# Performance work log

Hardware: AMD Instinct MI355X
Metric: run time of the kernel (lower is better)

The kernel has to match this reference:

```python
import jax, jax.numpy as jnp
import numpy as np

B, N = 2, 512
NEG = -1e9  # mask fill for masked max (self-loops guarantee >=1 neighbor)


def _dense_init(key, fan_in, fan_out):
    kw, kb = jax.random.split(key)
    scale = 1.0 / np.sqrt(fan_in)
    W = jax.random.normal(kw, (fan_in, fan_out), dtype=jnp.float32) * scale
    b = jnp.zeros((fan_out,), dtype=jnp.float32)
    return W, b


def setup_inputs() -> dict:
    key = jax.random.key(0)
    ks = jax.random.split(key, 16)
    coordinates = jax.random.normal(ks[0], (B, N, 3), dtype=jnp.float32)
    adjacency = (jax.random.uniform(ks[1], (B, N, N)) < 0.05).astype(jnp.float32)
    adjacency = jnp.maximum(adjacency, jnp.eye(N, dtype=jnp.float32)[None])
    node_features = jax.random.normal(ks[2], (B, N, 63), dtype=jnp.float32)
    center_scores = jax.random.uniform(ks[3], (B, N, 1), dtype=jnp.float32)

    W_h1, b_h1 = _dense_init(ks[4], 3, 64)
    W_h2, b_h2 = _dense_init(ks[5], 64, 64)
    # concat dim = 64 + 63 + 1 = 128; EdgeConv edge feature dim = 2 * F_in
    ec1_W1, ec1_b1 = _dense_init(ks[6], 256, 64)
    ec1_W2, ec1_b2 = _dense_init(ks[7], 64, 64)
    ec2_W1, ec2_b1 = _dense_init(ks[8], 128, 64)
    ec2_W2, ec2_b2 = _dense_init(ks[9], 64, 64)
    ec3_W1, ec3_b1 = _dense_init(ks[10], 128, 64)
    ec3_W2, ec3_b2 = _dense_init(ks[11], 64, 64)
    W_h6, b_h6 = _dense_init(ks[12], 64, 128)
    W_out, b_out = _dense_init(ks[13], 128, 3)
    return dict(coordinates=coordinates, adjacency=adjacency,
                node_features=node_features, center_scores=center_scores,
                W_h1=W_h1, b_h1=b_h1, W_h2=W_h2, b_h2=b_h2,
                ec1_W1=ec1_W1, ec1_b1=ec1_b1, ec1_W2=ec1_W2, ec1_b2=ec1_b2,
                ec2_W1=ec2_W1, ec2_b1=ec2_b1, ec2_W2=ec2_W2, ec2_b2=ec2_b2,
                ec3_W1=ec3_W1, ec3_b1=ec3_b1, ec3_W2=ec3_W2, ec3_b2=ec3_b2,
                W_h6=W_h6, b_h6=b_h6, W_out=W_out, b_out=b_out)


def _edge_conv(A, x, W1, b1, W2, b2):
    # DGCNN EdgeConv: m_ij = MLP([x_i, x_j - x_i]); out_i = max_{j in N(i)} m_ij
    Bn, Nn, F = x.shape
    xi = jnp.broadcast_to(x[:, :, None, :], (Bn, Nn, Nn, F))  # [B,N,N,F]
    xj = jnp.broadcast_to(x[:, None, :, :], (Bn, Nn, Nn, F))
    e = jnp.concatenate([xi, xj - xi], axis=-1)               # [B,N,N,2F]
    h = jax.nn.relu(jnp.einsum('bijf,fo->bijo', e, W1) + b1)
    h = jax.nn.relu(jnp.einsum('bijo,op->bijp', h, W2) + b2)
    h = jnp.where(A[..., None] > 0, h, NEG)
    return jnp.max(h, axis=2)                                  # [B,N,F_out]


def reference(coordinates, adjacency, node_features, center_scores,
              W_h1, b_h1, W_h2, b_h2,
              ec1_W1, ec1_b1, ec1_W2, ec1_b2,
              ec2_W1, ec2_b1, ec2_W2, ec2_b2,
              ec3_W1, ec3_b1, ec3_W2, ec3_b2,
              W_h6, b_h6, W_out, b_out):
    x = jax.nn.relu(coordinates @ W_h1 + b_h1)
    x = jax.nn.relu(x @ W_h2 + b_h2)
    x = jnp.concatenate([x, node_features, center_scores], axis=-1)  # [B,N,128]
    x = _edge_conv(adjacency, x, ec1_W1, ec1_b1, ec1_W2, ec1_b2)
    ec1_out = x
    x = _edge_conv(adjacency, x, ec2_W1, ec2_b1, ec2_W2, ec2_b2)
    ec2_out = x
    x = x + ec1_out
    x = _edge_conv(adjacency, x, ec3_W1, ec3_b1, ec3_W2, ec3_b2)
    x = x + ec2_out
    x = jax.nn.relu(x @ W_h6 + b_h6)
    x = jax.nn.relu(x @ W_out + b_out)
    return x
```

## Files before the change

### kernel.cpp

```cpp
#include <hip/hip_runtime.h>
#include <hip/hip_bf16.h>


#define NEGV -1e9f
#define MAXNBR 96

__device__ __forceinline__ float edge_partial(
    int beg, int myc, int o, const int* nbr, const float* __restrict__ vb,
    float ui, float bo, const float* wcol, float* hbuf) {
  float acc = NEGV;
  if (myc <= 0) return acc;
  float vl[4];
#pragma unroll
  for (int t = 0; t < 4; t++) {
    int e = t < myc ? t : myc - 1;
    vl[t] = vb[nbr[beg + e] * 64 + o];
  }
  for (int e0 = 0; e0 < myc; e0 += 4) {
    float4 hw;
    hw.x = fmaxf(ui + vl[0], 0.f);
    hw.y = fmaxf(ui + vl[1], 0.f);
    hw.z = fmaxf(ui + vl[2], 0.f);
    hw.w = fmaxf(ui + vl[3], 0.f);
    *(float4*)(hbuf + o * 4) = hw;
    if (e0 + 4 < myc) {
#pragma unroll
      for (int t = 0; t < 4; t++) {
        int e = e0 + 4 + t;
        if (e >= myc) e = myc - 1;
        vl[t] = vb[nbr[beg + e] * 64 + o];
      }
    }
    float s0 = bo, s1 = bo, s2 = bo, s3 = bo;
#pragma unroll
    for (int k = 0; k < 64; k++) {
      float4 hv = *(const float4*)(hbuf + k * 4);
      s0 = fmaf(hv.x, wcol[k], s0);
      s1 = fmaf(hv.y, wcol[k], s1);
      s2 = fmaf(hv.z, wcol[k], s2);
      s3 = fmaf(hv.w, wcol[k], s3);
    }
    acc = fmaxf(acc, fmaxf(s0, 0.f));
    if (e0 + 1 < myc) acc = fmaxf(acc, fmaxf(s1, 0.f));
    if (e0 + 2 < myc) acc = fmaxf(acc, fmaxf(s2, 0.f));
    if (e0 + 3 < myc) acc = fmaxf(acc, fmaxf(s3, 0.f));
  }
  return acc;
}

__global__ __launch_bounds__(64) void k1_node_uv(
    const float* __restrict__ coords, const float* __restrict__ A,
    const float* __restrict__ nf, const float* __restrict__ cs,
    const float* __restrict__ Wh1, const float* __restrict__ bh1,
    const float* __restrict__ Wh2, const float* __restrict__ bh2,
    const float* __restrict__ W1, const float* __restrict__ b1,
    float* __restrict__ u, float* __restrict__ v,
    int* __restrict__ nbrCnt, int* __restrict__ nbrG) {
  int node = blockIdx.x;
  int o = threadIdx.x;
  __shared__ float t[64];
  __shared__ float xs[128];
  {
    const float* Arow = A + (size_t)node * 512;
    int base = 0;
    for (int c = 0; c < 8; c++) {
      bool p = Arow[c * 64 + o] > 0.f;
      unsigned long long m = __ballot(p);
      if (p) {
        int pos = base + __builtin_popcountll(m & ((1ull << o) - 1ull));
        if (pos < MAXNBR) nbrG[node * MAXNBR + pos] = c * 64 + o;
      }
      base += __builtin_popcountll(m);
    }
    if (o == 0) nbrCnt[node] = base < MAXNBR ? base : MAXNBR;
  }
  float c0 = coords[node * 3 + 0];
  float c1 = coords[node * 3 + 1];
  float c2 = coords[node * 3 + 2];
  float a = bh1[o];
  a = fmaf(c0, Wh1[o], a);
  a = fmaf(c1, Wh1[64 + o], a);
  a = fmaf(c2, Wh1[128 + o], a);
  t[o] = fmaxf(a, 0.f);
  __syncthreads();
  float a2 = bh2[o];
#pragma unroll 8
  for (int k = 0; k < 64; k++) a2 = fmaf(t[k], Wh2[k * 64 + o], a2);
  xs[o] = fmaxf(a2, 0.f);
  if (o < 63) xs[64 + o] = nf[node * 63 + o];
  if (o == 63) xs[127] = cs[node];
  __syncthreads();
  float ua = b1[o], va = 0.f;
#pragma unroll 4
  for (int k = 0; k < 128; k++) {
    float xk = xs[k];
    float wt = W1[k * 64 + o];
    float wb = W1[(128 + k) * 64 + o];
    ua = fmaf(xk, wt - wb, ua);
    va = fmaf(xk, wb, va);
  }
  u[node * 64 + o] = ua;
  v[node * 64 + o] = va;
}

__global__ __launch_bounds__(128) void k_edgeconv_uv(
    const int* __restrict__ nbrCnt, const int* __restrict__ nbrG,
    const float* __restrict__ u, const float* __restrict__ v,
    const float* __restrict__ W2, const float* __restrict__ b2,
    const float* __restrict__ res,
    float* __restrict__ raw_out,
    const float* __restrict__ W1n, const float* __restrict__ b1n,
    float* __restrict__ un, float* __restrict__ vn) {
  __shared__ int s_nbr[MAXNBR];
  __shared__ float s_h[2][64 * 4];
  __shared__ float s_pm[2][64];
  __shared__ float s_xs[64];
  int row = blockIdx.x;
  int tid = threadIdx.x;
  int w = tid >> 6, o = tid & 63;
  int cnt = __builtin_amdgcn_readfirstlane(nbrCnt[row]);
  if (tid < MAXNBR) s_nbr[tid] = (tid < cnt) ? nbrG[row * MAXNBR + tid] : 0;
  float wcol[64];
#pragma unroll
  for (int k = 0; k < 64; k++) wcol[k] = W2[k * 64 + o];
  float ui = u[row * 64 + o];
  float bo = b2[o];
  const float* vb = v + (size_t)(row >> 9) * (512 * 64);
  __syncthreads();
  int half = (cnt + 1) >> 1;
  int beg = w ? half : 0;
  int myc = (w ? cnt : half) - beg;
  s_pm[w][o] = edge_partial(beg, myc, o, s_nbr, vb, ui, bo, wcol, s_h[w]);
  __syncthreads();
  float acc = fmaxf(s_pm[0][o], s_pm[1][o]);
  if (w == 0) {
    raw_out[row * 64 + o] = acc;
    s_xs[o] = acc + (res ? res[row * 64 + o] : 0.f);
  }
  __syncthreads();
  const float* Wb = W1n + 64 * 64;
  if (w == 0) {
    float a = b1n[o];
#pragma unroll 4
    for (int k = 0; k < 64; k++)
      a = fmaf(s_xs[k], W1n[k * 64 + o] - Wb[k * 64 + o], a);
    un[row * 64 + o] = a;
  } else {
    float a = 0.f;
#pragma unroll 4
    for (int k = 0; k < 64; k++) a = fmaf(s_xs[k], Wb[k * 64 + o], a);
    vn[row * 64 + o] = a;
  }
}

__global__ __launch_bounds__(128) void k_edgeconv_final(
    const int* __restrict__ nbrCnt, const int* __restrict__ nbrG,
    const float* __restrict__ u, const float* __restrict__ v,
    const float* __restrict__ W2, const float* __restrict__ b2,
    const float* __restrict__ res,
    const float* __restrict__ Wh6, const float* __restrict__ bh6,
    const float* __restrict__ Wout, const float* __restrict__ bout,
    float* __restrict__ out) {
  __shared__ int s_nbr[MAXNBR];
  __shared__ float s_h[2][64 * 4];
  __shared__ float s_pm[2][64];
  __shared__ float s_xs[64];
  __shared__ float s_h6[128];
  int row = blockIdx.x;
  int tid = threadIdx.x;
  int w = tid >> 6, o = tid & 63;
  int cnt = __builtin_amdgcn_readfirstlane(nbrCnt[row]);
  if (tid < MAXNBR) s_nbr[tid] = (tid < cnt) ? nbrG[row * MAXNBR + tid] : 0;
  float wcol[64];
#pragma unroll
  for (int k = 0; k < 64; k++) wcol[k] = W2[k * 64 + o];
  float ui = u[row * 64 + o];
  float bo = b2[o];
  const float* vb = v + (size_t)(row >> 9) * (512 * 64);
  __syncthreads();
  int half = (cnt + 1) >> 1;
  int beg = w ? half : 0;
  int myc = (w ? cnt : half) - beg;
  s_pm[w][o] = edge_partial(beg, myc, o, s_nbr, vb, ui, bo, wcol, s_h[w]);
  __syncthreads();
  if (w == 0) {
    float acc = fmaxf(s_pm[0][o], s_pm[1][o]);
    s_xs[o] = acc + res[row * 64 + o];
  }
  __syncthreads();
  {
    float s = bh6[tid];
#pragma unroll 4
    for (int k = 0; k < 64; k++) s = fmaf(s_xs[k], Wh6[k * 128 + tid], s);
    s_h6[tid] = fmaxf(s, 0.f);
  }
  __syncthreads();
  if (tid < 3) {
    float s = bout[tid];
#pragma unroll 8
    for (int k = 0; k < 128; k++) s = fmaf(s_h6[k], Wout[k * 3 + tid], s);
    out[row * 3 + tid] = fmaxf(s, 0.f);
  }
}

extern "C" void kernel_launch(void* const* d_in, const int* in_sizes, int n_in,
                              void* d_out, int out_size, void* d_ws,
                              size_t ws_size, hipStream_t stream) {
  const float* coords = (const float*)d_in[0];
  const float* A      = (const float*)d_in[1];
  const float* nf     = (const float*)d_in[2];
  const float* cs     = (const float*)d_in[3];
  const float* Wh1 = (const float*)d_in[4];
  const float* bh1 = (const float*)d_in[5];
  const float* Wh2 = (const float*)d_in[6];
  const float* bh2 = (const float*)d_in[7];
  const float* e1W1 = (const float*)d_in[8];
  const float* e1b1 = (const float*)d_in[9];
  const float* e1W2 = (const float*)d_in[10];
  const float* e1b2 = (const float*)d_in[11];
  const float* e2W1 = (const float*)d_in[12];
  const float* e2b1 = (const float*)d_in[13];
  const float* e2W2 = (const float*)d_in[14];
  const float* e2b2 = (const float*)d_in[15];
  const float* e3W1 = (const float*)d_in[16];
  const float* e3b1 = (const float*)d_in[17];
  const float* e3W2 = (const float*)d_in[18];
  const float* e3b2 = (const float*)d_in[19];
  const float* Wh6 = (const float*)d_in[20];
  const float* bh6 = (const float*)d_in[21];
  const float* Wout = (const float*)d_in[22];
  const float* bout = (const float*)d_in[23];

  float* ws = (float*)d_ws;
  float* u1  = ws + 0 * 65536;
  float* v1  = ws + 1 * 65536;
  float* e1o = ws + 2 * 65536;
  float* u2  = ws + 3 * 65536;
  float* v2  = ws + 4 * 65536;
  float* e2r = ws + 5 * 65536;
  float* u3  = ws + 6 * 65536;
  float* v3  = ws + 7 * 65536;
  int* wsI = (int*)(ws + 8 * 65536);
  int* nbrCnt = wsI;
  int* nbrG   = wsI + 1024;
  float* out = (float*)d_out;

  k1_node_uv<<<dim3(1024), dim3(64), 0, stream>>>(
      coords, A, nf, cs, Wh1, bh1, Wh2, bh2, e1W1, e1b1, u1, v1, nbrCnt, nbrG);
  k_edgeconv_uv<<<dim3(1024), dim3(128), 0, stream>>>(
      nbrCnt, nbrG, u1, v1, e1W2, e1b2, nullptr, e1o, e2W1, e2b1, u2, v2);
  k_edgeconv_uv<<<dim3(1024), dim3(128), 0, stream>>>(
      nbrCnt, nbrG, u2, v2, e2W2, e2b2, e1o, e2r, e3W1, e3b1, u3, v3);
  k_edgeconv_final<<<dim3(1024), dim3(128), 0, stream>>>(
      nbrCnt, nbrG, u3, v3, e3W2, e3b2, e2r, Wh6, bh6, Wout, bout, out);
}
```

Before: 159.3 us.

## Split edge neighbors across four waves and parallelize adjacency scan in node kernel

The EdgeConv kernels now launch 256 threads per row, so four wavefronts each take a quarter of the neighbor list instead of two waves taking halves. The four partial maxima are combined in shared memory. The first kernel moves to 128 threads: one wave builds the neighbor list with float4 adjacency loads while the other computes the node MLP and u/v projections concurrently. This shortens the per-row serial chain of 4-neighbor chunks and overlaps the adjacency scan with the MLP. In exchange, block size, shared memory and idle waves in the tail phases all grow, and the MLP wave now relies on wave-synchronous shared memory without barriers.

```diff
diff --git a/kernel.cpp b/kernel.cpp
--- a/kernel.cpp
+++ b/kernel.cpp
@@ -48,7 +48,7 @@
   return acc;
 }
 
-__global__ __launch_bounds__(64) void k1_node_uv(
+__global__ __launch_bounds__(128) void k1_node_uv(
     const float* __restrict__ coords, const float* __restrict__ A,
     const float* __restrict__ nf, const float* __restrict__ cs,
     const float* __restrict__ Wh1, const float* __restrict__ bh1,
@@ -57,53 +57,58 @@
     float* __restrict__ u, float* __restrict__ v,
     int* __restrict__ nbrCnt, int* __restrict__ nbrG) {
   int node = blockIdx.x;
-  int o = threadIdx.x;
+  int tid = threadIdx.x;
+  int w = tid >> 6, o = tid & 63;
   __shared__ float t[64];
   __shared__ float xs[128];
-  {
+  if (w == 1) {
     const float* Arow = A + (size_t)node * 512;
+    float4 a0 = *(const float4*)(Arow + o * 4);
+    float4 a1 = *(const float4*)(Arow + 256 + o * 4);
+    float av[8] = {a0.x, a0.y, a0.z, a0.w, a1.x, a1.y, a1.z, a1.w};
     int base = 0;
-    for (int c = 0; c < 8; c++) {
-      bool p = Arow[c * 64 + o] > 0.f;
+#pragma unroll
+    for (int j = 0; j < 8; j++) {
+      bool p = av[j] > 0.f;
       unsigned long long m = __ballot(p);
       if (p) {
         int pos = base + __builtin_popcountll(m & ((1ull << o) - 1ull));
-        if (pos < MAXNBR) nbrG[node * MAXNBR + pos] = c * 64 + o;
+        int col = (j < 4) ? (4 * o + j) : (256 + 4 * o + (j - 4));
+        if (pos < MAXNBR) nbrG[node * MAXNBR + pos] = col;
       }
       base += __builtin_popcountll(m);
     }
     if (o == 0) nbrCnt[node] = base < MAXNBR ? base : MAXNBR;
-  }
-  float c0 = coords[node * 3 + 0];
-  float c1 = coords[node * 3 + 1];
-  float c2 = coords[node * 3 + 2];
-  float a = bh1[o];
-  a = fmaf(c0, Wh1[o], a);
-  a = fmaf(c1, Wh1[64 + o], a);
-  a = fmaf(c2, Wh1[128 + o], a);
-  t[o] = fmaxf(a, 0.f);
-  __syncthreads();
-  float a2 = bh2[o];
+  } else {
+    float c0 = coords[node * 3 + 0];
+    float c1 = coords[node * 3 + 1];
+    float c2 = coords[node * 3 + 2];
+    float a = bh1[o];
+    a = fmaf(c0, Wh1[o], a);
+    a = fmaf(c1, Wh1[64 + o], a);
+    a = fmaf(c2, Wh1[128 + o], a);
+    t[o] = fmaxf(a, 0.f);
+    float a2 = bh2[o];
 #pragma unroll 8
-  for (int k = 0; k < 64; k++) a2 = fmaf(t[k], Wh2[k * 64 + o], a2);
-  xs[o] = fmaxf(a2, 0.f);
-  if (o < 63) xs[64 + o] = nf[node * 63 + o];
-  if (o == 63) xs[127] = cs[node];
-  __syncthreads();
-  float ua = b1[o], va = 0.f;
-#pragma unroll 4
-  for (int k = 0; k < 128; k++) {
-    float xk = xs[k];
-    float wt = W1[k * 64 + o];
-    float wb = W1[(128 + k) * 64 + o];
-    ua = fmaf(xk, wt - wb, ua);
-    va = fmaf(xk, wb, va);
-  }
-  u[node * 64 + o] = ua;
-  v[node * 64 + o] = va;
-}
-
-__global__ __launch_bounds__(128) void k_edgeconv_uv(
+    for (int k = 0; k < 64; k++) a2 = fmaf(t[k], Wh2[k * 64 + o], a2);
+    xs[o] = fmaxf(a2, 0.f);
+    if (o < 63) xs[64 + o] = nf[node * 63 + o];
+    if (o == 63) xs[127] = cs[node];
+    float ua = b1[o], va = 0.f;
+#pragma unroll 4
+    for (int k = 0; k < 128; k++) {
+      float xk = xs[k];
+      float wt = W1[k * 64 + o];
+      float wb = W1[(128 + k) * 64 + o];
+      ua = fmaf(xk, wt - wb, ua);
+      va = fmaf(xk, wb, va);
+    }
+    u[node * 64 + o] = ua;
+    v[node * 64 + o] = va;
+  }
+}
+
+__global__ __launch_bounds__(256) void k_edgeconv_uv(
     const int* __restrict__ nbrCnt, const int* __restrict__ nbrG,
     const float* __restrict__ u, const float* __restrict__ v,
     const float* __restrict__ W2, const float* __restrict__ b2,
@@ -112,8 +117,8 @@
     const float* __restrict__ W1n, const float* __restrict__ b1n,
     float* __restrict__ un, float* __restrict__ vn) {
   __shared__ int s_nbr[MAXNBR];
-  __shared__ float s_h[2][64 * 4];
-  __shared__ float s_pm[2][64];
+  __shared__ float s_h[4][64 * 4];
+  __shared__ float s_pm[4][64];
   __shared__ float s_xs[64];
   int row = blockIdx.x;
   int tid = threadIdx.x;
@@ -127,13 +132,16 @@
   float bo = b2[o];
   const float* vb = v + (size_t)(row >> 9) * (512 * 64);
   __syncthreads();
-  int half = (cnt + 1) >> 1;
-  int beg = w ? half : 0;
-  int myc = (w ? cnt : half) - beg;
-  s_pm[w][o] = edge_partial(beg, myc, o, s_nbr, vb, ui, bo, wcol, s_h[w]);
-  __syncthreads();
-  float acc = fmaxf(s_pm[0][o], s_pm[1][o]);
+  int q = (cnt + 3) >> 2;
+  int beg = w * q;
+  if (beg > cnt) beg = cnt;
+  int end = beg + q;
+  if (end > cnt) end = cnt;
+  s_pm[w][o] = edge_partial(beg, end - beg, o, s_nbr, vb, ui, bo, wcol, s_h[w]);
+  __syncthreads();
   if (w == 0) {
+    float acc = fmaxf(fmaxf(s_pm[0][o], s_pm[1][o]),
+                      fmaxf(s_pm[2][o], s_pm[3][o]));
     raw_out[row * 64 + o] = acc;
     s_xs[o] = acc + (res ? res[row * 64 + o] : 0.f);
   }
@@ -145,7 +153,7 @@
     for (int k = 0; k < 64; k++)
       a = fmaf(s_xs[k], W1n[k * 64 + o] - Wb[k * 64 + o], a);
     un[row * 64 + o] = a;
-  } else {
+  } else if (w == 1) {
     float a = 0.f;
 #pragma unroll 4
     for (int k = 0; k < 64; k++) a = fmaf(s_xs[k], Wb[k * 64 + o], a);
@@ -153,7 +161,7 @@
   }
 }
 
-__global__ __launch_bounds__(128) void k_edgeconv_final(
+__global__ __launch_bounds__(256) void k_edgeconv_final(
     const int* __restrict__ nbrCnt, const int* __restrict__ nbrG,
     const float* __restrict__ u, const float* __restrict__ v,
     const float* __restrict__ W2, const float* __restrict__ b2,
@@ -162,8 +170,8 @@
     const float* __restrict__ Wout, const float* __restrict__ bout,
     float* __restrict__ out) {
   __shared__ int s_nbr[MAXNBR];
-  __shared__ float s_h[2][64 * 4];
-  __shared__ float s_pm[2][64];
+  __shared__ float s_h[4][64 * 4];
+  __shared__ float s_pm[4][64];
   __shared__ float s_xs[64];
   __shared__ float s_h6[128];
   int row = blockIdx.x;
@@ -178,17 +186,20 @@
   float bo = b2[o];
   const float* vb = v + (size_t)(row >> 9) * (512 * 64);
   __syncthreads();
-  int half = (cnt + 1) >> 1;
-  int beg = w ? half : 0;
-  int myc = (w ? cnt : half) - beg;
-  s_pm[w][o] = edge_partial(beg, myc, o, s_nbr, vb, ui, bo, wcol, s_h[w]);
+  int q = (cnt + 3) >> 2;
+  int beg = w * q;
+  if (beg > cnt) beg = cnt;
+  int end = beg + q;
+  if (end > cnt) end = cnt;
+  s_pm[w][o] = edge_partial(beg, end - beg, o, s_nbr, vb, ui, bo, wcol, s_h[w]);
   __syncthreads();
   if (w == 0) {
-    float acc = fmaxf(s_pm[0][o], s_pm[1][o]);
+    float acc = fmaxf(fmaxf(s_pm[0][o], s_pm[1][o]),
+                      fmaxf(s_pm[2][o], s_pm[3][o]));
     s_xs[o] = acc + res[row * 64 + o];
   }
   __syncthreads();
-  {
+  if (tid < 128) {
     float s = bh6[tid];
 #pragma unroll 4
     for (int k = 0; k < 64; k++) s = fmaf(s_xs[k], Wh6[k * 128 + tid], s);
@@ -245,12 +256,12 @@
   int* nbrG   = wsI + 1024;
   float* out = (float*)d_out;
 
-  k1_node_uv<<<dim3(1024), dim3(64), 0, stream>>>(
+  k1_node_uv<<<dim3(1024), dim3(128), 0, stream>>>(
       coords, A, nf, cs, Wh1, bh1, Wh2, bh2, e1W1, e1b1, u1, v1, nbrCnt, nbrG);
-  k_edgeconv_uv<<<dim3(1024), dim3(128), 0, stream>>>(
+  k_edgeconv_uv<<<dim3(1024), dim3(256), 0, stream>>>(
       nbrCnt, nbrG, u1, v1, e1W2, e1b2, nullptr, e1o, e2W1, e2b1, u2, v2);
-  k_edgeconv_uv<<<dim3(1024), dim3(128), 0, stream>>>(
+  k_edgeconv_uv<<<dim3(1024), dim3(256), 0, stream>>>(
       nbrCnt, nbrG, u2, v2, e2W2, e2b2, e1o, e2r, e3W1, e3b1, u3, v3);
-  k_edgeconv_final<<<dim3(1024), dim3(128), 0, stream>>>(
+  k_edgeconv_final<<<dim3(1024), dim3(256), 0, stream>>>(
       nbrCnt, nbrG, u3, v3, e3W2, e3b2, e2r, Wh6, bh6, Wout, bout, out);
 }
```

New measurement: 152.2 us. -4.4%, faster.
